# Kernel optimization log

Measured on AMD Instinct MI355X. Metric: run time of the kernel, lower is better.

## Reference

```python
import jax, jax.numpy as jnp
import numpy as np
import math

N_AGENTS = 16

def _mlp2(x, W1, b1, W2, b2):
    # tanh on first layer only, matching the torch module
    return jnp.tanh(x @ W1 + b1) @ W2 + b2

def setup_inputs() -> dict:
    key = jax.random.key(0)
    ks = jax.random.split(key, 24)
    B, N, A, IN, D = 2048, N_AGENTS, 32, 128, 128
    NODES = B * N
    s = 0.05
    inp = {
        "obs": jax.random.normal(ks[0], (NODES, IN), jnp.float32),
        "policies": jax.random.uniform(ks[1], (NODES, A), jnp.float32),
        "actions": jax.random.uniform(ks[2], (NODES, A), jnp.float32),
        "weights": jax.random.uniform(ks[3], (1,), jnp.float32),
        "noise": jax.random.normal(ks[4], (NODES, N, A), jnp.float32) * 0.1,
        "Wk1": jax.random.normal(ks[5], (IN, 32), jnp.float32) * s,
        "bk1": jnp.zeros((32,), jnp.float32),
        "Wk2": jax.random.normal(ks[6], (32, D), jnp.float32) * s,
        "bk2": jnp.zeros((D,), jnp.float32),
        "Wq1": jax.random.normal(ks[7], (IN, 32), jnp.float32) * s,
        "bq1": jnp.zeros((32,), jnp.float32),
        "Wq2": jax.random.normal(ks[8], (32, D), jnp.float32) * s,
        "bq2": jnp.zeros((D,), jnp.float32),
        "Wv1": jax.random.normal(ks[9], (IN, 32), jnp.float32) * s,
        "bv1": jnp.zeros((32,), jnp.float32),
        "Wv2": jax.random.normal(ks[10], (32, D), jnp.float32) * s,
        "bv2": jnp.zeros((D,), jnp.float32),
        "Wval": jax.random.normal(ks[11], (D + A, 1), jnp.float32) * s,
        "bval": jnp.zeros((1,), jnp.float32),
    }
    return inp

def reference(obs, policies, actions, weights, noise,
              Wk1, bk1, Wk2, bk2, Wq1, bq1, Wq2, bq2, Wv1, bv1, Wv2, bv2,
              Wval, bval):
    N = N_AGENTS
    NODES, _ = obs.shape
    B = NODES // N
    A = policies.shape[-1]
    D = Wk2.shape[1]

    # ---- SoftAttentionInput: graph soft attention over complete N-agent graphs
    k = _mlp2(obs, Wk1, bk1, Wk2, bk2).reshape(B, N, D)
    q = _mlp2(obs, Wq1, bq1, Wq2, bq2).reshape(B, N, D)
    v = _mlp2(obs, Wv1, bv1, Wv2, bv2).reshape(B, N, D)
    # score for receiver i from sender j: key[j] . query[i]
    scores = jnp.einsum('bjd,bid->bij', k, q) / math.sqrt(D)
    alpha = jax.nn.softmax(scores, axis=-1)               # softmax over senders j
    obs_proc = jnp.einsum('bij,bjd->bid', alpha, v)       # [B,N,D]

    # ---- SoftAttentionWeight: PRD mixing of policies and noisy actions
    pi = policies.reshape(B, N, A)
    act = actions.reshape(B, N, A)
    w = weights                                           # scalar mixing weight, shape (1,)
    # z[b,i,k] = w*act[b,k] + (1-w)*pi[b,k] + noise (mailbox of receiver i)
    z = w * act[:, None, :, :] + (1.0 - w) * pi[:, None, :, :] + noise.reshape(B, N, N, A)
    # place_policies construction: z_final[b,i,j,k] = pi[b,k] if k==j else z[b,i,k];
    # mean over k  =>  (pi[b,j] - z[b,i,j] + sum_k z[b,i,k]) / N
    z_sum = jnp.sum(z, axis=2)                            # [B,N,A]
    z_mix = (pi[:, None, :, :] - z + z_sum[:, :, None, :]) / N  # [B,i,j,A]

    obs_b = jnp.broadcast_to(obs_proc[:, None, :, :], (B, N, N, D))  # [b,i,j] = obs_proc[b,j]
    obs_final = jnp.concatenate([obs_b, z_mix], axis=-1).reshape(B * N, N, D + A)

    # ---- ValueNetwork
    x = obs_final @ Wval + bval                           # [B*N, N, 1]
    weights_preproc = alpha.reshape(B * N, N, 1)
    return x, weights_preproc
```

## Files before the change

### kernel.cpp

```cpp
#include <hip/hip_runtime.h>

typedef __attribute__((ext_vector_type(8))) short bf16x8;
typedef __attribute__((ext_vector_type(4))) float f32x4;

__device__ __forceinline__ unsigned short f2bf(float f){
  union { float f; unsigned int u; } v; v.f = f;
  unsigned int u = v.u;
  return (unsigned short)((u + 0x7FFFu + ((u >> 16) & 1u)) >> 16);
}

__device__ __forceinline__ float fast_tanh(float x){
  x = fminf(15.f, fmaxf(-15.f, x));
  float e = __expf(2.f * x);
  return (e - 1.f) / (e + 1.f);
}

__device__ __forceinline__ float dot128(const float* __restrict__ a,
                                        const float* __restrict__ b){
  float s = 0.f;
  for (int c = 0; c < 128; c += 4){
    float4 x = *(const float4*)(a + c);
    float4 y = *(const float4*)(b + c);
    s += x.x*y.x + x.y*y.y + x.z*y.z + x.w*y.w;
  }
  return s;
}

#define GRPSUM(x) { x += __shfl_xor(x, 1); x += __shfl_xor(x, 2); \
                    x += __shfl_xor(x, 4); x += __shfl_xor(x, 8); }

__global__ __launch_bounds__(64) void k0_kernel(
    const float* __restrict__ Wk1, const float* __restrict__ Wq1, const float* __restrict__ Wv1,
    const float* __restrict__ Wk2, const float* __restrict__ bk2,
    const float* __restrict__ Wq2, const float* __restrict__ bq2,
    const float* __restrict__ Wv2, const float* __restrict__ bv2,
    const float* __restrict__ Wval, float* __restrict__ ws)
{
  const int tid = blockIdx.x * 64 + threadIdx.x;
  const float rs = 0.08838834764831845f;
  unsigned short* bp = (unsigned short*)ws;
  unsigned short* b2 = (unsigned short*)(ws + 6144);

  if (tid < 1536){
    const int e = tid & 7, l = (tid >> 3) & 63, tt = tid >> 9;
    const int g = (l >> 4) * 8 + e;
    float val = 0.f;
    if (tt < 2){
      const int h = (l & 15) + tt * 16;
      val = rs * dot128(Wk2 + h * 128, Wq2 + g * 128);
    } else if ((l & 15) == 0){
      val = rs * dot128(Wq2 + g * 128, bk2);
    }
    b2[tid] = f2bf(val);
  } else if (tid < 1600){
    const int h = tid - 1536;
    if (h < 32) ws[6912 + h] = rs * dot128(Wk2 + h * 128, bq2);
    else        ws[6944 + (h - 32)] = dot128(Wv2 + (h - 32) * 128, Wval);
  } else if (tid == 1600){
    ws[6976] = rs * dot128(bk2, bq2);
  } else if (tid == 1601){
    ws[6977] = dot128(bv2, Wval);
  }

  for (int idx = tid; idx < 12288; idx += 4096){
    const int e  = idx & 7;
    const int l  = (idx >> 3) & 63;
    const int kc = (idx >> 9) & 3;
    const int nt = (idx >> 11) & 1;
    const int m  = idx >> 12;
    const float* W1 = (m == 0) ? Wk1 : ((m == 1) ? Wq1 : Wv1);
    const int krow = kc * 32 + (l >> 4) * 8 + e;
    const int col  = nt * 16 + (l & 15);
    bp[idx] = f2bf(W1[krow * 32 + col]);
  }
}

__global__ __launch_bounds__(256, 2) void fused_kernel(
    const float* __restrict__ obs,
    const float* __restrict__ policies, const float* __restrict__ actions,
    const float* __restrict__ noise, const float* __restrict__ weights,
    const float* __restrict__ bk1p, const float* __restrict__ bq1p, const float* __restrict__ bv1p,
    const float* __restrict__ Wval, const float* __restrict__ bval,
    const float* __restrict__ ws,
    float* __restrict__ out_x, float* __restrict__ out_alpha)
{
  __shared__ __align__(16) unsigned short hk_s[4][512];
  __shared__ __align__(16) unsigned short hq_s[4][512];
  __shared__ __align__(16) unsigned short tq_s[4][512];
  __shared__ __align__(16) float rql_s[4][16];
  __shared__ __align__(16) float vvl_s[4][16];
  __shared__ __align__(16) float nvw_s[4][256];
  __shared__ __align__(16) float pvl_s[4][16], avl_s[4][16], ovl_s[4][16];

  const int t = threadIdx.x;
  const int wid = t >> 6, l = t & 63;
  const int b = blockIdx.x * 4 + wid;
  const int li = l & 15, gp = l >> 4;

  const float* orow = obs + (size_t)(b * 16 + li) * 128 + gp * 8;
  float4 ob[8];
#pragma unroll
  for (int kc = 0; kc < 4; kc++){
    ob[kc * 2]     = *(const float4*)(orow + kc * 32);
    ob[kc * 2 + 1] = *(const float4*)(orow + kc * 32 + 4);
  }

  const int q8 = l & 7, r8 = l >> 3;
  const float* nb = noise + (size_t)b * 8192 + r8 * 32 + q8 * 4;
  float4 nzA[8], nzB[8];
#pragma unroll
  for (int p = 0; p < 8; p++) nzA[p] = *(const float4*)(nb + p * 256);

  const int jp = l >> 2, seg = l & 3;
  const float* pp = policies + (size_t)(b * 16 + jp) * 32 + seg * 8;
  const float* ap = actions  + (size_t)(b * 16 + jp) * 32 + seg * 8;
  float4 pA0 = *(const float4*)(pp);
  float4 pA1 = *(const float4*)(pp + 4);
  float4 aA0 = *(const float4*)(ap);
  float4 aA1 = *(const float4*)(ap + 4);
  const float4 wpa = *(const float4*)(Wval + 128 + seg * 8);
  const float4 wpb = *(const float4*)(Wval + 132 + seg * 8);
  const float4 wv4 = *(const float4*)(Wval + 128 + q8 * 4);

  const bf16x8* bp  = (const bf16x8*)ws;
  const bf16x8* b2p = (const bf16x8*)(ws + 6144);
  const bf16x8 b20 = b2p[l], b21 = b2p[64 + l], b22 = b2p[128 + l];
  const float u0 = ws[6912 + li], u1 = ws[6928 + li];
  const float wv0 = ws[6944 + li], wv1 = ws[6960 + li];
  const float ccv = ws[6976], cvv = ws[6977];
  const float bk0 = bk1p[li], bk1v = bk1p[16 + li];
  const float bq0 = bq1p[li], bq1v = bq1p[16 + li];
  const float bv0 = bv1p[li], bv1v = bv1p[16 + li];
  const float wscal = weights[0];
  const float bvs = bval[0];

  bf16x8 afr[4];
#pragma unroll
  for (int kc = 0; kc < 4; kc++){
    bf16x8 a;
    a[0]=(short)f2bf(ob[kc*2].x); a[1]=(short)f2bf(ob[kc*2].y);
    a[2]=(short)f2bf(ob[kc*2].z); a[3]=(short)f2bf(ob[kc*2].w);
    a[4]=(short)f2bf(ob[kc*2+1].x); a[5]=(short)f2bf(ob[kc*2+1].y);
    a[6]=(short)f2bf(ob[kc*2+1].z); a[7]=(short)f2bf(ob[kc*2+1].w);
    afr[kc] = a;
  }
  f32x4 acc[6];
#pragma unroll
  for (int mt = 0; mt < 6; mt++){ f32x4 z = {0.f,0.f,0.f,0.f}; acc[mt] = z; }
#pragma unroll
  for (int mt = 0; mt < 6; mt++){
#pragma unroll
    for (int kc = 0; kc < 4; kc++)
      acc[mt] = __builtin_amdgcn_mfma_f32_16x16x32_bf16(afr[kc], bp[(mt*4+kc)*64 + l], acc[mt], 0, 0, 0);
  }

  unsigned short* hkb = hk_s[wid];
  unsigned short* hqb = hq_s[wid];
#pragma unroll
  for (int tile = 0; tile < 2; tile++){
    const float bk_ = tile ? bk1v : bk0;
    const float bq_ = tile ? bq1v : bq0;
    f32x4 ck = acc[tile], cq = acc[2 + tile];
#pragma unroll
    for (int r = 0; r < 4; r++){
      hkb[(gp*4+r)*32 + tile*16 + li] = f2bf(fast_tanh(ck[r] + bk_));
      hqb[(gp*4+r)*32 + tile*16 + li] = f2bf(fast_tanh(cq[r] + bq_));
    }
  }

  {
    f32x4 c0 = acc[4], c1 = acc[5];
    float vp0 = wv0*fast_tanh(c0[0]+bv0) + wv1*fast_tanh(c1[0]+bv1v);
    float vp1 = wv0*fast_tanh(c0[1]+bv0) + wv1*fast_tanh(c1[1]+bv1v);
    float vp2 = wv0*fast_tanh(c0[2]+bv0) + wv1*fast_tanh(c1[2]+bv1v);
    float vp3 = wv0*fast_tanh(c0[3]+bv0) + wv1*fast_tanh(c1[3]+bv1v);
    GRPSUM(vp0); GRPSUM(vp1); GRPSUM(vp2); GRPSUM(vp3);
    if (li == 0){
      float4 vq; vq.x = vp0+cvv; vq.y = vp1+cvv; vq.z = vp2+cvv; vq.w = vp3+cvv;
      *(float4*)&vvl_s[wid][gp*4] = vq;
    }
  }

#pragma unroll
  for (int p = 0; p < 8; p++) nzB[p] = *(const float4*)(nb + 2048 + p * 256);
  float* nvw = nvw_s[wid];
#pragma unroll
  for (int p = 0; p < 8; p++){
    float s = nzA[p].x*wv4.x + nzA[p].y*wv4.y + nzA[p].z*wv4.z + nzA[p].w*wv4.w;
    s += __shfl_xor(s, 1); s += __shfl_xor(s, 2); s += __shfl_xor(s, 4);
    if (q8 == 0) nvw[p * 8 + r8] = s;
  }
#pragma unroll
  for (int p = 0; p < 8; p++) nzA[p] = *(const float4*)(nb + 4096 + p * 256);

  const bf16x8 aq = *(const bf16x8*)(hqb + li*32 + gp*8);
  f32x4 cu0 = {u0,u0,u0,u0}, cu1 = {u1,u1,u1,u1}, cu2 = {ccv,ccv,ccv,ccv};
  f32x4 tq0 = __builtin_amdgcn_mfma_f32_16x16x32_bf16(aq, b20, cu0, 0, 0, 0);
  f32x4 tq1 = __builtin_amdgcn_mfma_f32_16x16x32_bf16(aq, b21, cu1, 0, 0, 0);
  f32x4 rqt = __builtin_amdgcn_mfma_f32_16x16x32_bf16(aq, b22, cu2, 0, 0, 0);
  if (li == 0){
    float4 rv; rv.x = rqt[0]; rv.y = rqt[1]; rv.z = rqt[2]; rv.w = rqt[3];
    *(float4*)&rql_s[wid][gp*4] = rv;
  }
  unsigned short* tqb = tq_s[wid];
#pragma unroll
  for (int r = 0; r < 4; r++){
    tqb[(gp*4+r)*32 + li]      = f2bf(tq0[r]);
    tqb[(gp*4+r)*32 + 16 + li] = f2bf(tq1[r]);
  }

  const bf16x8 ak = *(const bf16x8*)(hkb + li*32 + gp*8);
  const bf16x8 bt = *(const bf16x8*)(tqb + li*32 + gp*8);
  f32x4 zz = {0.f,0.f,0.f,0.f};
  f32x4 S = __builtin_amdgcn_mfma_f32_16x16x32_bf16(ak, bt, zz, 0, 0, 0);
  const float rc = rql_s[wid][li];
  float s0 = S[0]+rc, s1 = S[1]+rc, s2 = S[2]+rc, s3 = S[3]+rc;

  float mx = fmaxf(fmaxf(s0, s1), fmaxf(s2, s3));
  mx = fmaxf(mx, __shfl_xor(mx, 16)); mx = fmaxf(mx, __shfl_xor(mx, 32));
  float e0 = __expf(s0-mx), e1 = __expf(s1-mx), e2 = __expf(s2-mx), e3 = __expf(s3-mx);
  float sm = e0+e1+e2+e3;
  sm += __shfl_xor(sm, 16); sm += __shfl_xor(sm, 32);
  const float inv = 1.f / sm;
  const float a0 = e0*inv, a1 = e1*inv, a2 = e2*inv, a3 = e3*inv;

  float* aT = (float*)tqb;
  { float4 av4; av4.x = a0; av4.y = a1; av4.z = a2; av4.w = a3;
    *(float4*)&aT[li*16 + gp*4] = av4; }
  { float4 o4 = *(const float4*)&aT[l*4];
    *(float4*)(out_alpha + (size_t)b*256 + l*4) = o4; }

  float4 vq4 = *(const float4*)&vvl_s[wid][gp*4];
  float ovp = a0*vq4.x + a1*vq4.y + a2*vq4.z + a3*vq4.w;
  ovp += __shfl_xor(ovp, 16); ovp += __shfl_xor(ovp, 32);
  if (l < 16) ovl_s[wid][li] = ovp;

#pragma unroll
  for (int p = 0; p < 8; p++){
    float s = nzB[p].x*wv4.x + nzB[p].y*wv4.y + nzB[p].z*wv4.z + nzB[p].w*wv4.w;
    s += __shfl_xor(s, 1); s += __shfl_xor(s, 2); s += __shfl_xor(s, 4);
    if (q8 == 0) nvw[64 + p * 8 + r8] = s;
  }
#pragma unroll
  for (int p = 0; p < 8; p++) nzB[p] = *(const float4*)(nb + 6144 + p * 256);

  {
    float pvv = pA0.x*wpa.x + pA0.y*wpa.y + pA0.z*wpa.z + pA0.w*wpa.w
              + pA1.x*wpb.x + pA1.y*wpb.y + pA1.z*wpb.z + pA1.w*wpb.w;
    float avv = aA0.x*wpa.x + aA0.y*wpa.y + aA0.z*wpa.z + aA0.w*wpa.w
              + aA1.x*wpb.x + aA1.y*wpb.y + aA1.z*wpb.z + aA1.w*wpb.w;
    pvv += __shfl_xor(pvv, 1); pvv += __shfl_xor(pvv, 2);
    avv += __shfl_xor(avv, 1); avv += __shfl_xor(avv, 2);
    if (seg == 0){ pvl_s[wid][jp] = pvv; avl_s[wid][jp] = avv; }
  }

#pragma unroll
  for (int p = 0; p < 8; p++){
    float s = nzA[p].x*wv4.x + nzA[p].y*wv4.y + nzA[p].z*wv4.z + nzA[p].w*wv4.w;
    s += __shfl_xor(s, 1); s += __shfl_xor(s, 2); s += __shfl_xor(s, 4);
    if (q8 == 0) nvw[128 + p * 8 + r8] = s;
  }
#pragma unroll
  for (int p = 0; p < 8; p++){
    float s = nzB[p].x*wv4.x + nzB[p].y*wv4.y + nzB[p].z*wv4.z + nzB[p].w*wv4.w;
    s += __shfl_xor(s, 1); s += __shfl_xor(s, 2); s += __shfl_xor(s, 4);
    if (q8 == 0) nvw[192 + p * 8 + r8] = s;
  }

  {
    const int j0 = (l & 3) * 4;
    const int ii = l >> 2;
    float4 pv4 = *(const float4*)&pvl_s[wid][j0];
    float4 av4 = *(const float4*)&avl_s[wid][j0];
    float4 ov4 = *(const float4*)&ovl_s[wid][j0];
    float4 nv4 = *(const float4*)&nvw[ii * 16 + j0];
    const float om = 1.f - wscal;
    float z0 = wscal * av4.x + om * pv4.x + nv4.x;
    float z1 = wscal * av4.y + om * pv4.y + nv4.y;
    float z2 = wscal * av4.z + om * pv4.z + nv4.z;
    float z3 = wscal * av4.w + om * pv4.w + nv4.w;
    float zs = z0 + z1 + z2 + z3;
    zs += __shfl_xor(zs, 1); zs += __shfl_xor(zs, 2);
    float4 o;
    o.x = ov4.x + (pv4.x - z0 + zs) * 0.0625f + bvs;
    o.y = ov4.y + (pv4.y - z1 + zs) * 0.0625f + bvs;
    o.z = ov4.z + (pv4.z - z2 + zs) * 0.0625f + bvs;
    o.w = ov4.w + (pv4.w - z3 + zs) * 0.0625f + bvs;
    *(float4*)(out_x + (size_t)b * 256 + l * 4) = o;
  }
}

extern "C" void kernel_launch(void* const* d_in, const int* in_sizes, int n_in,
                              void* d_out, int out_size, void* d_ws, size_t ws_size,
                              hipStream_t stream)
{
  const float* obs      = (const float*)d_in[0];
  const float* policies = (const float*)d_in[1];
  const float* actions  = (const float*)d_in[2];
  const float* weights  = (const float*)d_in[3];
  const float* noise    = (const float*)d_in[4];
  const float* Wk1  = (const float*)d_in[5];
  const float* bk1  = (const float*)d_in[6];
  const float* Wk2  = (const float*)d_in[7];
  const float* bk2  = (const float*)d_in[8];
  const float* Wq1  = (const float*)d_in[9];
  const float* bq1  = (const float*)d_in[10];
  const float* Wq2  = (const float*)d_in[11];
  const float* bq2  = (const float*)d_in[12];
  const float* Wv1  = (const float*)d_in[13];
  const float* bv1  = (const float*)d_in[14];
  const float* Wv2  = (const float*)d_in[15];
  const float* bv2  = (const float*)d_in[16];
  const float* Wval = (const float*)d_in[17];
  const float* bval = (const float*)d_in[18];

  float* out = (float*)d_out;
  float* ws  = (float*)d_ws;

  const int NODES = in_sizes[0] / 128;
  const int B = NODES / 16;

  float* out_x     = out;
  float* out_alpha = out + (size_t)NODES * 16;

  hipLaunchKernelGGL(k0_kernel, dim3(64), dim3(64), 0, stream,
                     Wk1, Wq1, Wv1, Wk2, bk2, Wq2, bq2, Wv2, bv2, Wval, ws);
  hipLaunchKernelGGL(fused_kernel, dim3(B / 4), dim3(256), 0, stream,
                     obs, policies, actions, noise, weights,
                     bk1, bq1, bv1, Wval, bval, ws,
                     out_x, out_alpha);
}
```

Measured before the change: 30.80 us.

## Split per-graph work across warps: one warp attention, three warps noise reduction

Rather than each warp handling a whole graph, one block now processes one graph. Warp 0 runs the MLP and attention MFMAs, while warps 1-3 share the noise-row dot products with Wval and the policy/action projections. A block barrier joins them before a 256-thread final combine. This raises the block count and spreads the noise-load latency, which dominates memory traffic, across more warps. The cost is an added __syncthreads and warp 0 now serialising its attention work against the others.

```diff
diff --git a/kernel.cpp b/kernel.cpp
--- a/kernel.cpp
+++ b/kernel.cpp
@@ -75,7 +75,7 @@
   }
 }
 
-__global__ __launch_bounds__(256, 2) void fused_kernel(
+__global__ __launch_bounds__(256, 2) void fused2_kernel(
     const float* __restrict__ obs,
     const float* __restrict__ policies, const float* __restrict__ actions,
     const float* __restrict__ noise, const float* __restrict__ weights,
@@ -84,209 +84,182 @@
     const float* __restrict__ ws,
     float* __restrict__ out_x, float* __restrict__ out_alpha)
 {
-  __shared__ __align__(16) unsigned short hk_s[4][512];
-  __shared__ __align__(16) unsigned short hq_s[4][512];
-  __shared__ __align__(16) unsigned short tq_s[4][512];
-  __shared__ __align__(16) float rql_s[4][16];
-  __shared__ __align__(16) float vvl_s[4][16];
-  __shared__ __align__(16) float nvw_s[4][256];
-  __shared__ __align__(16) float pvl_s[4][16], avl_s[4][16], ovl_s[4][16];
+  __shared__ __align__(16) unsigned short hk_s[512];
+  __shared__ __align__(16) unsigned short hq_s[512];
+  __shared__ __align__(16) unsigned short tq_s[512];
+  __shared__ __align__(16) float rql_s[16];
+  __shared__ __align__(16) float vvl_s[16];
+  __shared__ __align__(16) float nvw[256];
+  __shared__ __align__(16) float pvl_s[16], avl_s[16], ovl_s[16];
 
   const int t = threadIdx.x;
   const int wid = t >> 6, l = t & 63;
-  const int b = blockIdx.x * 4 + wid;
-  const int li = l & 15, gp = l >> 4;
-
-  const float* orow = obs + (size_t)(b * 16 + li) * 128 + gp * 8;
-  float4 ob[8];
-#pragma unroll
-  for (int kc = 0; kc < 4; kc++){
-    ob[kc * 2]     = *(const float4*)(orow + kc * 32);
-    ob[kc * 2 + 1] = *(const float4*)(orow + kc * 32 + 4);
-  }
-
-  const int q8 = l & 7, r8 = l >> 3;
-  const float* nb = noise + (size_t)b * 8192 + r8 * 32 + q8 * 4;
-  float4 nzA[8], nzB[8];
-#pragma unroll
-  for (int p = 0; p < 8; p++) nzA[p] = *(const float4*)(nb + p * 256);
-
-  const int jp = l >> 2, seg = l & 3;
-  const float* pp = policies + (size_t)(b * 16 + jp) * 32 + seg * 8;
-  const float* ap = actions  + (size_t)(b * 16 + jp) * 32 + seg * 8;
-  float4 pA0 = *(const float4*)(pp);
-  float4 pA1 = *(const float4*)(pp + 4);
-  float4 aA0 = *(const float4*)(ap);
-  float4 aA1 = *(const float4*)(ap + 4);
-  const float4 wpa = *(const float4*)(Wval + 128 + seg * 8);
-  const float4 wpb = *(const float4*)(Wval + 132 + seg * 8);
-  const float4 wv4 = *(const float4*)(Wval + 128 + q8 * 4);
-
-  const bf16x8* bp  = (const bf16x8*)ws;
-  const bf16x8* b2p = (const bf16x8*)(ws + 6144);
-  const bf16x8 b20 = b2p[l], b21 = b2p[64 + l], b22 = b2p[128 + l];
-  const float u0 = ws[6912 + li], u1 = ws[6928 + li];
-  const float wv0 = ws[6944 + li], wv1 = ws[6960 + li];
-  const float ccv = ws[6976], cvv = ws[6977];
-  const float bk0 = bk1p[li], bk1v = bk1p[16 + li];
-  const float bq0 = bq1p[li], bq1v = bq1p[16 + li];
-  const float bv0 = bv1p[li], bv1v = bv1p[16 + li];
+  const int b = blockIdx.x;
   const float wscal = weights[0];
   const float bvs = bval[0];
 
-  bf16x8 afr[4];
-#pragma unroll
-  for (int kc = 0; kc < 4; kc++){
-    bf16x8 a;
-    a[0]=(short)f2bf(ob[kc*2].x); a[1]=(short)f2bf(ob[kc*2].y);
-    a[2]=(short)f2bf(ob[kc*2].z); a[3]=(short)f2bf(ob[kc*2].w);
-    a[4]=(short)f2bf(ob[kc*2+1].x); a[5]=(short)f2bf(ob[kc*2+1].y);
-    a[6]=(short)f2bf(ob[kc*2+1].z); a[7]=(short)f2bf(ob[kc*2+1].w);
-    afr[kc] = a;
-  }
-  f32x4 acc[6];
-#pragma unroll
-  for (int mt = 0; mt < 6; mt++){ f32x4 z = {0.f,0.f,0.f,0.f}; acc[mt] = z; }
-#pragma unroll
-  for (int mt = 0; mt < 6; mt++){
-#pragma unroll
-    for (int kc = 0; kc < 4; kc++)
-      acc[mt] = __builtin_amdgcn_mfma_f32_16x16x32_bf16(afr[kc], bp[(mt*4+kc)*64 + l], acc[mt], 0, 0, 0);
-  }
-
-  unsigned short* hkb = hk_s[wid];
-  unsigned short* hqb = hq_s[wid];
-#pragma unroll
-  for (int tile = 0; tile < 2; tile++){
-    const float bk_ = tile ? bk1v : bk0;
-    const float bq_ = tile ? bq1v : bq0;
-    f32x4 ck = acc[tile], cq = acc[2 + tile];
+  if (wid == 0){
+    const int li = l & 15, gp = l >> 4;
+
+    const float* orow = obs + (size_t)(b * 16 + li) * 128 + gp * 8;
+    float4 ob[8];
+#pragma unroll
+    for (int kc = 0; kc < 4; kc++){
+      ob[kc * 2]     = *(const float4*)(orow + kc * 32);
+      ob[kc * 2 + 1] = *(const float4*)(orow + kc * 32 + 4);
+    }
+
+    const bf16x8* bp  = (const bf16x8*)ws;
+    const bf16x8* b2p = (const bf16x8*)(ws + 6144);
+    const bf16x8 b20 = b2p[l], b21 = b2p[64 + l], b22 = b2p[128 + l];
+    const float u0 = ws[6912 + li], u1 = ws[6928 + li];
+    const float wv0 = ws[6944 + li], wv1 = ws[6960 + li];
+    const float ccv = ws[6976], cvv = ws[6977];
+    const float bk0 = bk1p[li], bk1v = bk1p[16 + li];
+    const float bq0 = bq1p[li], bq1v = bq1p[16 + li];
+    const float bv0 = bv1p[li], bv1v = bv1p[16 + li];
+
+    bf16x8 afr[4];
+#pragma unroll
+    for (int kc = 0; kc < 4; kc++){
+      bf16x8 a;
+      a[0]=(short)f2bf(ob[kc*2].x); a[1]=(short)f2bf(ob[kc*2].y);
+      a[2]=(short)f2bf(ob[kc*2].z); a[3]=(short)f2bf(ob[kc*2].w);
+      a[4]=(short)f2bf(ob[kc*2+1].x); a[5]=(short)f2bf(ob[kc*2+1].y);
+      a[6]=(short)f2bf(ob[kc*2+1].z); a[7]=(short)f2bf(ob[kc*2+1].w);
+      afr[kc] = a;
+    }
+    f32x4 acc[6];
+#pragma unroll
+    for (int mt = 0; mt < 6; mt++){ f32x4 z = {0.f,0.f,0.f,0.f}; acc[mt] = z; }
+#pragma unroll
+    for (int mt = 0; mt < 6; mt++){
+#pragma unroll
+      for (int kc = 0; kc < 4; kc++)
+        acc[mt] = __builtin_amdgcn_mfma_f32_16x16x32_bf16(afr[kc], bp[(mt*4+kc)*64 + l], acc[mt], 0, 0, 0);
+    }
+
+#pragma unroll
+    for (int tile = 0; tile < 2; tile++){
+      const float bk_ = tile ? bk1v : bk0;
+      const float bq_ = tile ? bq1v : bq0;
+      f32x4 ck = acc[tile], cq = acc[2 + tile];
+#pragma unroll
+      for (int r = 0; r < 4; r++){
+        hk_s[(gp*4+r)*32 + tile*16 + li] = f2bf(fast_tanh(ck[r] + bk_));
+        hq_s[(gp*4+r)*32 + tile*16 + li] = f2bf(fast_tanh(cq[r] + bq_));
+      }
+    }
+
+    {
+      f32x4 c0 = acc[4], c1 = acc[5];
+      float vp0 = wv0*fast_tanh(c0[0]+bv0) + wv1*fast_tanh(c1[0]+bv1v);
+      float vp1 = wv0*fast_tanh(c0[1]+bv0) + wv1*fast_tanh(c1[1]+bv1v);
+      float vp2 = wv0*fast_tanh(c0[2]+bv0) + wv1*fast_tanh(c1[2]+bv1v);
+      float vp3 = wv0*fast_tanh(c0[3]+bv0) + wv1*fast_tanh(c1[3]+bv1v);
+      GRPSUM(vp0); GRPSUM(vp1); GRPSUM(vp2); GRPSUM(vp3);
+      if (li == 0){
+        float4 vq; vq.x = vp0+cvv; vq.y = vp1+cvv; vq.z = vp2+cvv; vq.w = vp3+cvv;
+        *(float4*)&vvl_s[gp*4] = vq;
+      }
+    }
+
+    const bf16x8 aq = *(const bf16x8*)(hq_s + li*32 + gp*8);
+    f32x4 cu0 = {u0,u0,u0,u0}, cu1 = {u1,u1,u1,u1}, cu2 = {ccv,ccv,ccv,ccv};
+    f32x4 tq0 = __builtin_amdgcn_mfma_f32_16x16x32_bf16(aq, b20, cu0, 0, 0, 0);
+    f32x4 tq1 = __builtin_amdgcn_mfma_f32_16x16x32_bf16(aq, b21, cu1, 0, 0, 0);
+    f32x4 rqt = __builtin_amdgcn_mfma_f32_16x16x32_bf16(aq, b22, cu2, 0, 0, 0);
+    if (li == 0){
+      float4 rv; rv.x = rqt[0]; rv.y = rqt[1]; rv.z = rqt[2]; rv.w = rqt[3];
+      *(float4*)&rql_s[gp*4] = rv;
+    }
 #pragma unroll
     for (int r = 0; r < 4; r++){
-      hkb[(gp*4+r)*32 + tile*16 + li] = f2bf(fast_tanh(ck[r] + bk_));
-      hqb[(gp*4+r)*32 + tile*16 + li] = f2bf(fast_tanh(cq[r] + bq_));
-    }
-  }
+      tq_s[(gp*4+r)*32 + li]      = f2bf(tq0[r]);
+      tq_s[(gp*4+r)*32 + 16 + li] = f2bf(tq1[r]);
+    }
+
+    const bf16x8 ak = *(const bf16x8*)(hk_s + li*32 + gp*8);
+    const bf16x8 bt = *(const bf16x8*)(tq_s + li*32 + gp*8);
+    f32x4 zz = {0.f,0.f,0.f,0.f};
+    f32x4 S = __builtin_amdgcn_mfma_f32_16x16x32_bf16(ak, bt, zz, 0, 0, 0);
+    const float rc = rql_s[li];
+    float s0 = S[0]+rc, s1 = S[1]+rc, s2 = S[2]+rc, s3 = S[3]+rc;
+
+    float mx = fmaxf(fmaxf(s0, s1), fmaxf(s2, s3));
+    mx = fmaxf(mx, __shfl_xor(mx, 16)); mx = fmaxf(mx, __shfl_xor(mx, 32));
+    float e0 = __expf(s0-mx), e1 = __expf(s1-mx), e2 = __expf(s2-mx), e3 = __expf(s3-mx);
+    float sm = e0+e1+e2+e3;
+    sm += __shfl_xor(sm, 16); sm += __shfl_xor(sm, 32);
+    const float inv = 1.f / sm;
+    const float a0 = e0*inv, a1 = e1*inv, a2 = e2*inv, a3 = e3*inv;
+
+    float* aT = (float*)tq_s;
+    { float4 av4; av4.x = a0; av4.y = a1; av4.z = a2; av4.w = a3;
+      *(float4*)&aT[li*16 + gp*4] = av4; }
+    { float4 o4 = *(const float4*)&aT[l*4];
+      *(float4*)(out_alpha + (size_t)b*256 + l*4) = o4; }
+
+    float4 vq4 = *(const float4*)&vvl_s[gp*4];
+    float ovp = a0*vq4.x + a1*vq4.y + a2*vq4.z + a3*vq4.w;
+    ovp += __shfl_xor(ovp, 16); ovp += __shfl_xor(ovp, 32);
+    if (l < 16) ovl_s[l] = ovp;
+  } else {
+    const int wn = wid - 1;
+    const int q8 = l & 7, r8 = l >> 3;
+    const int rbase = wn * 88 + r8;
+    const float* nb = noise + (size_t)b * 8192;
+    const float4 wv4 = *(const float4*)(Wval + 128 + q8 * 4);
+
+    float4 pA0, pA1, aA0, aA1, wpa, wpb;
+    const int jp = l >> 2, seg = l & 3;
+    if (wid == 1){
+      const float* pp = policies + (size_t)(b * 16 + jp) * 32 + seg * 8;
+      const float* ap = actions  + (size_t)(b * 16 + jp) * 32 + seg * 8;
+      pA0 = *(const float4*)(pp);
+      pA1 = *(const float4*)(pp + 4);
+      aA0 = *(const float4*)(ap);
+      aA1 = *(const float4*)(ap + 4);
+      wpa = *(const float4*)(Wval + 128 + seg * 8);
+      wpb = *(const float4*)(Wval + 132 + seg * 8);
+    }
+
+    float4 nz[11];
+#pragma unroll
+    for (int p = 0; p < 11; p++){
+      const int row = rbase + p * 8;
+      if (row < 256) nz[p] = *(const float4*)(nb + row * 32 + q8 * 4);
+    }
+#pragma unroll
+    for (int p = 0; p < 11; p++){
+      const int row = rbase + p * 8;
+      if (row < 256){
+        float s = nz[p].x*wv4.x + nz[p].y*wv4.y + nz[p].z*wv4.z + nz[p].w*wv4.w;
+        s += __shfl_xor(s, 1); s += __shfl_xor(s, 2); s += __shfl_xor(s, 4);
+        if (q8 == 0) nvw[row] = s;
+      }
+    }
+
+    if (wid == 1){
+      float pvv = pA0.x*wpa.x + pA0.y*wpa.y + pA0.z*wpa.z + pA0.w*wpa.w
+                + pA1.x*wpb.x + pA1.y*wpb.y + pA1.z*wpb.z + pA1.w*wpb.w;
+      float avv = aA0.x*wpa.x + aA0.y*wpa.y + aA0.z*wpa.z + aA0.w*wpa.w
+                + aA1.x*wpb.x + aA1.y*wpb.y + aA1.z*wpb.z + aA1.w*wpb.w;
+      pvv += __shfl_xor(pvv, 1); pvv += __shfl_xor(pvv, 2);
+      avv += __shfl_xor(avv, 1); avv += __shfl_xor(avv, 2);
+      if (seg == 0){ pvl_s[jp] = pvv; avl_s[jp] = avv; }
+    }
+  }
+
+  __syncthreads();
 
   {
-    f32x4 c0 = acc[4], c1 = acc[5];
-    float vp0 = wv0*fast_tanh(c0[0]+bv0) + wv1*fast_tanh(c1[0]+bv1v);
-    float vp1 = wv0*fast_tanh(c0[1]+bv0) + wv1*fast_tanh(c1[1]+bv1v);
-    float vp2 = wv0*fast_tanh(c0[2]+bv0) + wv1*fast_tanh(c1[2]+bv1v);
-    float vp3 = wv0*fast_tanh(c0[3]+bv0) + wv1*fast_tanh(c1[3]+bv1v);
-    GRPSUM(vp0); GRPSUM(vp1); GRPSUM(vp2); GRPSUM(vp3);
-    if (li == 0){
-      float4 vq; vq.x = vp0+cvv; vq.y = vp1+cvv; vq.z = vp2+cvv; vq.w = vp3+cvv;
-      *(float4*)&vvl_s[wid][gp*4] = vq;
-    }
-  }
-
-#pragma unroll
-  for (int p = 0; p < 8; p++) nzB[p] = *(const float4*)(nb + 2048 + p * 256);
-  float* nvw = nvw_s[wid];
-#pragma unroll
-  for (int p = 0; p < 8; p++){
-    float s = nzA[p].x*wv4.x + nzA[p].y*wv4.y + nzA[p].z*wv4.z + nzA[p].w*wv4.w;
-    s += __shfl_xor(s, 1); s += __shfl_xor(s, 2); s += __shfl_xor(s, 4);
-    if (q8 == 0) nvw[p * 8 + r8] = s;
-  }
-#pragma unroll
-  for (int p = 0; p < 8; p++) nzA[p] = *(const float4*)(nb + 4096 + p * 256);
-
-  const bf16x8 aq = *(const bf16x8*)(hqb + li*32 + gp*8);
-  f32x4 cu0 = {u0,u0,u0,u0}, cu1 = {u1,u1,u1,u1}, cu2 = {ccv,ccv,ccv,ccv};
-  f32x4 tq0 = __builtin_amdgcn_mfma_f32_16x16x32_bf16(aq, b20, cu0, 0, 0, 0);
-  f32x4 tq1 = __builtin_amdgcn_mfma_f32_16x16x32_bf16(aq, b21, cu1, 0, 0, 0);
-  f32x4 rqt = __builtin_amdgcn_mfma_f32_16x16x32_bf16(aq, b22, cu2, 0, 0, 0);
-  if (li == 0){
-    float4 rv; rv.x = rqt[0]; rv.y = rqt[1]; rv.z = rqt[2]; rv.w = rqt[3];
-    *(float4*)&rql_s[wid][gp*4] = rv;
-  }
-  unsigned short* tqb = tq_s[wid];
-#pragma unroll
-  for (int r = 0; r < 4; r++){
-    tqb[(gp*4+r)*32 + li]      = f2bf(tq0[r]);
-    tqb[(gp*4+r)*32 + 16 + li] = f2bf(tq1[r]);
-  }
-
-  const bf16x8 ak = *(const bf16x8*)(hkb + li*32 + gp*8);
-  const bf16x8 bt = *(const bf16x8*)(tqb + li*32 + gp*8);
-  f32x4 zz = {0.f,0.f,0.f,0.f};
-  f32x4 S = __builtin_amdgcn_mfma_f32_16x16x32_bf16(ak, bt, zz, 0, 0, 0);
-  const float rc = rql_s[wid][li];
-  float s0 = S[0]+rc, s1 = S[1]+rc, s2 = S[2]+rc, s3 = S[3]+rc;
-
-  float mx = fmaxf(fmaxf(s0, s1), fmaxf(s2, s3));
-  mx = fmaxf(mx, __shfl_xor(mx, 16)); mx = fmaxf(mx, __shfl_xor(mx, 32));
-  float e0 = __expf(s0-mx), e1 = __expf(s1-mx), e2 = __expf(s2-mx), e3 = __expf(s3-mx);
-  float sm = e0+e1+e2+e3;
-  sm += __shfl_xor(sm, 16); sm += __shfl_xor(sm, 32);
-  const float inv = 1.f / sm;
-  const float a0 = e0*inv, a1 = e1*inv, a2 = e2*inv, a3 = e3*inv;
-
-  float* aT = (float*)tqb;
-  { float4 av4; av4.x = a0; av4.y = a1; av4.z = a2; av4.w = a3;
-    *(float4*)&aT[li*16 + gp*4] = av4; }
-  { float4 o4 = *(const float4*)&aT[l*4];
-    *(float4*)(out_alpha + (size_t)b*256 + l*4) = o4; }
-
-  float4 vq4 = *(const float4*)&vvl_s[wid][gp*4];
-  float ovp = a0*vq4.x + a1*vq4.y + a2*vq4.z + a3*vq4.w;
-  ovp += __shfl_xor(ovp, 16); ovp += __shfl_xor(ovp, 32);
-  if (l < 16) ovl_s[wid][li] = ovp;
-
-#pragma unroll
-  for (int p = 0; p < 8; p++){
-    float s = nzB[p].x*wv4.x + nzB[p].y*wv4.y + nzB[p].z*wv4.z + nzB[p].w*wv4.w;
-    s += __shfl_xor(s, 1); s += __shfl_xor(s, 2); s += __shfl_xor(s, 4);
-    if (q8 == 0) nvw[64 + p * 8 + r8] = s;
-  }
-#pragma unroll
-  for (int p = 0; p < 8; p++) nzB[p] = *(const float4*)(nb + 6144 + p * 256);
-
-  {
-    float pvv = pA0.x*wpa.x + pA0.y*wpa.y + pA0.z*wpa.z + pA0.w*wpa.w
-              + pA1.x*wpb.x + pA1.y*wpb.y + pA1.z*wpb.z + pA1.w*wpb.w;
-    float avv = aA0.x*wpa.x + aA0.y*wpa.y + aA0.z*wpa.z + aA0.w*wpa.w
-              + aA1.x*wpb.x + aA1.y*wpb.y + aA1.z*wpb.z + aA1.w*wpb.w;
-    pvv += __shfl_xor(pvv, 1); pvv += __shfl_xor(pvv, 2);
-    avv += __shfl_xor(avv, 1); avv += __shfl_xor(avv, 2);
-    if (seg == 0){ pvl_s[wid][jp] = pvv; avl_s[wid][jp] = avv; }
-  }
-
-#pragma unroll
-  for (int p = 0; p < 8; p++){
-    float s = nzA[p].x*wv4.x + nzA[p].y*wv4.y + nzA[p].z*wv4.z + nzA[p].w*wv4.w;
-    s += __shfl_xor(s, 1); s += __shfl_xor(s, 2); s += __shfl_xor(s, 4);
-    if (q8 == 0) nvw[128 + p * 8 + r8] = s;
-  }
-#pragma unroll
-  for (int p = 0; p < 8; p++){
-    float s = nzB[p].x*wv4.x + nzB[p].y*wv4.y + nzB[p].z*wv4.z + nzB[p].w*wv4.w;
-    s += __shfl_xor(s, 1); s += __shfl_xor(s, 2); s += __shfl_xor(s, 4);
-    if (q8 == 0) nvw[192 + p * 8 + r8] = s;
-  }
-
-  {
-    const int j0 = (l & 3) * 4;
-    const int ii = l >> 2;
-    float4 pv4 = *(const float4*)&pvl_s[wid][j0];
-    float4 av4 = *(const float4*)&avl_s[wid][j0];
-    float4 ov4 = *(const float4*)&ovl_s[wid][j0];
-    float4 nv4 = *(const float4*)&nvw[ii * 16 + j0];
-    const float om = 1.f - wscal;
-    float z0 = wscal * av4.x + om * pv4.x + nv4.x;
-    float z1 = wscal * av4.y + om * pv4.y + nv4.y;
-    float z2 = wscal * av4.z + om * pv4.z + nv4.z;
-    float z3 = wscal * av4.w + om * pv4.w + nv4.w;
-    float zs = z0 + z1 + z2 + z3;
-    zs += __shfl_xor(zs, 1); zs += __shfl_xor(zs, 2);
-    float4 o;
-    o.x = ov4.x + (pv4.x - z0 + zs) * 0.0625f + bvs;
-    o.y = ov4.y + (pv4.y - z1 + zs) * 0.0625f + bvs;
-    o.z = ov4.z + (pv4.z - z2 + zs) * 0.0625f + bvs;
-    o.w = ov4.w + (pv4.w - z3 + zs) * 0.0625f + bvs;
-    *(float4*)(out_x + (size_t)b * 256 + l * 4) = o;
+    const int j = t & 15;
+    const float pv = pvl_s[j], av = avl_s[j];
+    const float zval = wscal * av + (1.f - wscal) * pv + nvw[t];
+    float zs = zval;
+    GRPSUM(zs);
+    out_x[(size_t)b * 256 + t] = ovl_s[t >> 4] + (pv - zval + zs) * 0.0625f + bvs;
   }
 }
 
@@ -325,7 +298,7 @@
 
   hipLaunchKernelGGL(k0_kernel, dim3(64), dim3(64), 0, stream,
                      Wk1, Wq1, Wv1, Wk2, bk2, Wq2, bq2, Wv2, bv2, Wval, ws);
-  hipLaunchKernelGGL(fused_kernel, dim3(B / 4), dim3(256), 0, stream,
+  hipLaunchKernelGGL(fused2_kernel, dim3(B), dim3(256), 0, stream,
                      obs, policies, actions, noise, weights,
                      bk1, bq1, bv1, Wval, bval, ws,
                      out_x, out_alpha);
```

Measured after the change: 32.02 us. 4.0% more time.

## Split noise/policy mixing into separate wide kernel, attention kernel adds onto output

Applied to the files above, without the earlier changes.

Moves the noise reduction and policy/action mixing part of the value output out of the fused attention kernel into the prologue kernel. That kernel now launches one 256-thread block per batch (plus four weight-prep blocks). The attention kernel then reads the partial output and adds the attention-value term. This spreads the bandwidth-heavy noise streaming (the largest input) across many more blocks and cuts register pressure in the attention kernel. In exchange it adds an extra global write and read of out_x and makes the second kernel depend on the first one finishing.

```diff
diff --git a/kernel.cpp b/kernel.cpp
--- a/kernel.cpp
+++ b/kernel.cpp
@@ -29,58 +29,131 @@
 #define GRPSUM(x) { x += __shfl_xor(x, 1); x += __shfl_xor(x, 2); \
                     x += __shfl_xor(x, 4); x += __shfl_xor(x, 8); }
 
-__global__ __launch_bounds__(64) void k0_kernel(
+
+__global__ __launch_bounds__(256) void kn_kernel(
+    const float* __restrict__ policies, const float* __restrict__ actions,
+    const float* __restrict__ noise, const float* __restrict__ weights,
+    const float* __restrict__ Wval, const float* __restrict__ bval,
     const float* __restrict__ Wk1, const float* __restrict__ Wq1, const float* __restrict__ Wv1,
     const float* __restrict__ Wk2, const float* __restrict__ bk2,
     const float* __restrict__ Wq2, const float* __restrict__ bq2,
     const float* __restrict__ Wv2, const float* __restrict__ bv2,
-    const float* __restrict__ Wval, float* __restrict__ ws)
+    float* __restrict__ ws, float* __restrict__ out_x)
 {
-  const int tid = blockIdx.x * 64 + threadIdx.x;
-  const float rs = 0.08838834764831845f;
-  unsigned short* bp = (unsigned short*)ws;
-  unsigned short* b2 = (unsigned short*)(ws + 6144);
-
-  if (tid < 1536){
-    const int e = tid & 7, l = (tid >> 3) & 63, tt = tid >> 9;
-    const int g = (l >> 4) * 8 + e;
-    float val = 0.f;
-    if (tt < 2){
-      const int h = (l & 15) + tt * 16;
-      val = rs * dot128(Wk2 + h * 128, Wq2 + g * 128);
-    } else if ((l & 15) == 0){
-      val = rs * dot128(Wq2 + g * 128, bk2);
+  const int t = threadIdx.x;
+
+  if ((int)blockIdx.x < 4){
+    const int tid2 = blockIdx.x * 256 + t;
+    const float rs = 0.08838834764831845f;
+    unsigned short* bp = (unsigned short*)ws;
+    unsigned short* b2 = (unsigned short*)(ws + 6144);
+
+    for (int d = tid2; d < 1602; d += 1024){
+      if (d < 1536){
+        const int e = d & 7, l = (d >> 3) & 63, tt = d >> 9;
+        const int g = (l >> 4) * 8 + e;
+        float val = 0.f;
+        if (tt < 2){
+          const int h = (l & 15) + tt * 16;
+          val = rs * dot128(Wk2 + h * 128, Wq2 + g * 128);
+        } else if ((l & 15) == 0){
+          val = rs * dot128(Wq2 + g * 128, bk2);
+        }
+        b2[d] = f2bf(val);
+      } else if (d < 1600){
+        const int h = d - 1536;
+        if (h < 32) ws[6912 + h] = rs * dot128(Wk2 + h * 128, bq2);
+        else        ws[6944 + (h - 32)] = dot128(Wv2 + (h - 32) * 128, Wval);
+      } else if (d == 1600){
+        ws[6976] = rs * dot128(bk2, bq2);
+      } else {
+        ws[6977] = dot128(bv2, Wval);
+      }
     }
-    b2[tid] = f2bf(val);
-  } else if (tid < 1600){
-    const int h = tid - 1536;
-    if (h < 32) ws[6912 + h] = rs * dot128(Wk2 + h * 128, bq2);
-    else        ws[6944 + (h - 32)] = dot128(Wv2 + (h - 32) * 128, Wval);
-  } else if (tid == 1600){
-    ws[6976] = rs * dot128(bk2, bq2);
-  } else if (tid == 1601){
-    ws[6977] = dot128(bv2, Wval);
-  }
-
-  for (int idx = tid; idx < 12288; idx += 4096){
-    const int e  = idx & 7;
-    const int l  = (idx >> 3) & 63;
-    const int kc = (idx >> 9) & 3;
-    const int nt = (idx >> 11) & 1;
-    const int m  = idx >> 12;
-    const float* W1 = (m == 0) ? Wk1 : ((m == 1) ? Wq1 : Wv1);
-    const int krow = kc * 32 + (l >> 4) * 8 + e;
-    const int col  = nt * 16 + (l & 15);
-    bp[idx] = f2bf(W1[krow * 32 + col]);
-  }
-}
-
-__global__ __launch_bounds__(256, 2) void fused_kernel(
+    for (int idx = tid2; idx < 12288; idx += 1024){
+      const int e  = idx & 7;
+      const int l  = (idx >> 3) & 63;
+      const int kc = (idx >> 9) & 3;
+      const int nt = (idx >> 11) & 1;
+      const int m  = idx >> 12;
+      const float* W1 = (m == 0) ? Wk1 : ((m == 1) ? Wq1 : Wv1);
+      const int krow = kc * 32 + (l >> 4) * 8 + e;
+      const int col  = nt * 16 + (l & 15);
+      bp[idx] = f2bf(W1[krow * 32 + col]);
+    }
+    return;
+  }
+
+  __shared__ __align__(16) float nvw[256];
+  __shared__ __align__(16) float pvl[16], avl[16];
+
+  const int b = blockIdx.x - 4;
+  const int w = t >> 6, l = t & 63;
+  const int q8 = l & 7, r8 = l >> 3;
+  const float4 wv4 = *(const float4*)(Wval + 128 + q8 * 4);
+
+  float4 pA0, pA1, aA0, aA1, wpa, wpb;
+  const int jp = l >> 2, seg = l & 3;
+  if (w == 0){
+    const float* pp = policies + (size_t)(b * 16 + jp) * 32 + seg * 8;
+    const float* ap = actions  + (size_t)(b * 16 + jp) * 32 + seg * 8;
+    pA0 = *(const float4*)(pp);
+    pA1 = *(const float4*)(pp + 4);
+    aA0 = *(const float4*)(ap);
+    aA1 = *(const float4*)(ap + 4);
+    wpa = *(const float4*)(Wval + 128 + seg * 8);
+    wpb = *(const float4*)(Wval + 132 + seg * 8);
+  }
+
+  const float* nbl = noise + (size_t)b * 8192 + (w * 64 + r8) * 32 + q8 * 4;
+  float4 nz[8];
+#pragma unroll
+  for (int p = 0; p < 8; p++) nz[p] = *(const float4*)(nbl + p * 256);
+#pragma unroll
+  for (int p = 0; p < 8; p++){
+    float s = nz[p].x*wv4.x + nz[p].y*wv4.y + nz[p].z*wv4.z + nz[p].w*wv4.w;
+    s += __shfl_xor(s, 1); s += __shfl_xor(s, 2); s += __shfl_xor(s, 4);
+    if (q8 == 0) nvw[w * 64 + p * 8 + r8] = s;
+  }
+
+  if (w == 0){
+    float pvv = pA0.x*wpa.x + pA0.y*wpa.y + pA0.z*wpa.z + pA0.w*wpa.w
+              + pA1.x*wpb.x + pA1.y*wpb.y + pA1.z*wpb.z + pA1.w*wpb.w;
+    float avv = aA0.x*wpa.x + aA0.y*wpa.y + aA0.z*wpa.z + aA0.w*wpa.w
+              + aA1.x*wpb.x + aA1.y*wpb.y + aA1.z*wpb.z + aA1.w*wpb.w;
+    pvv += __shfl_xor(pvv, 1); pvv += __shfl_xor(pvv, 2);
+    avv += __shfl_xor(avv, 1); avv += __shfl_xor(avv, 2);
+    if (seg == 0){ pvl[jp] = pvv; avl[jp] = avv; }
+  }
+
+  __syncthreads();
+
+  if (w == 0){
+    const float wscal = weights[0];
+    const float bvs = bval[0];
+    const int i = l >> 2, j0 = (l & 3) * 4;
+    float4 pv4 = *(const float4*)&pvl[j0];
+    float4 av4 = *(const float4*)&avl[j0];
+    float4 nv4 = *(const float4*)&nvw[i * 16 + j0];
+    const float om = 1.f - wscal;
+    float z0 = wscal * av4.x + om * pv4.x + nv4.x;
+    float z1 = wscal * av4.y + om * pv4.y + nv4.y;
+    float z2 = wscal * av4.z + om * pv4.z + nv4.z;
+    float z3 = wscal * av4.w + om * pv4.w + nv4.w;
+    float zs = z0 + z1 + z2 + z3;
+    zs += __shfl_xor(zs, 1); zs += __shfl_xor(zs, 2);
+    float4 o;
+    o.x = (pv4.x - z0 + zs) * 0.0625f + bvs;
+    o.y = (pv4.y - z1 + zs) * 0.0625f + bvs;
+    o.z = (pv4.z - z2 + zs) * 0.0625f + bvs;
+    o.w = (pv4.w - z3 + zs) * 0.0625f + bvs;
+    *(float4*)(out_x + (size_t)b * 256 + l * 4) = o;
+  }
+}
+
+__global__ __launch_bounds__(256) void ka_kernel(
     const float* __restrict__ obs,
-    const float* __restrict__ policies, const float* __restrict__ actions,
-    const float* __restrict__ noise, const float* __restrict__ weights,
     const float* __restrict__ bk1p, const float* __restrict__ bq1p, const float* __restrict__ bv1p,
-    const float* __restrict__ Wval, const float* __restrict__ bval,
     const float* __restrict__ ws,
     float* __restrict__ out_x, float* __restrict__ out_alpha)
 {
@@ -89,8 +162,7 @@
   __shared__ __align__(16) unsigned short tq_s[4][512];
   __shared__ __align__(16) float rql_s[4][16];
   __shared__ __align__(16) float vvl_s[4][16];
-  __shared__ __align__(16) float nvw_s[4][256];
-  __shared__ __align__(16) float pvl_s[4][16], avl_s[4][16], ovl_s[4][16];
+  __shared__ __align__(16) float ovl_s[4][16];
 
   const int t = threadIdx.x;
   const int wid = t >> 6, l = t & 63;
@@ -104,23 +176,7 @@
     ob[kc * 2]     = *(const float4*)(orow + kc * 32);
     ob[kc * 2 + 1] = *(const float4*)(orow + kc * 32 + 4);
   }
-
-  const int q8 = l & 7, r8 = l >> 3;
-  const float* nb = noise + (size_t)b * 8192 + r8 * 32 + q8 * 4;
-  float4 nzA[8], nzB[8];
-#pragma unroll
-  for (int p = 0; p < 8; p++) nzA[p] = *(const float4*)(nb + p * 256);
-
-  const int jp = l >> 2, seg = l & 3;
-  const float* pp = policies + (size_t)(b * 16 + jp) * 32 + seg * 8;
-  const float* ap = actions  + (size_t)(b * 16 + jp) * 32 + seg * 8;
-  float4 pA0 = *(const float4*)(pp);
-  float4 pA1 = *(const float4*)(pp + 4);
-  float4 aA0 = *(const float4*)(ap);
-  float4 aA1 = *(const float4*)(ap + 4);
-  const float4 wpa = *(const float4*)(Wval + 128 + seg * 8);
-  const float4 wpb = *(const float4*)(Wval + 132 + seg * 8);
-  const float4 wv4 = *(const float4*)(Wval + 128 + q8 * 4);
+  float4 x4 = *(const float4*)(out_x + (size_t)b * 256 + l * 4);
 
   const bf16x8* bp  = (const bf16x8*)ws;
   const bf16x8* b2p = (const bf16x8*)(ws + 6144);
@@ -131,8 +187,6 @@
   const float bk0 = bk1p[li], bk1v = bk1p[16 + li];
   const float bq0 = bq1p[li], bq1v = bq1p[16 + li];
   const float bv0 = bv1p[li], bv1v = bv1p[16 + li];
-  const float wscal = weights[0];
-  const float bvs = bval[0];
 
   bf16x8 afr[4];
 #pragma unroll
@@ -181,18 +235,6 @@
     }
   }
 
-#pragma unroll
-  for (int p = 0; p < 8; p++) nzB[p] = *(const float4*)(nb + 2048 + p * 256);
-  float* nvw = nvw_s[wid];
-#pragma unroll
-  for (int p = 0; p < 8; p++){
-    float s = nzA[p].x*wv4.x + nzA[p].y*wv4.y + nzA[p].z*wv4.z + nzA[p].w*wv4.w;
-    s += __shfl_xor(s, 1); s += __shfl_xor(s, 2); s += __shfl_xor(s, 4);
-    if (q8 == 0) nvw[p * 8 + r8] = s;
-  }
-#pragma unroll
-  for (int p = 0; p < 8; p++) nzA[p] = *(const float4*)(nb + 4096 + p * 256);
-
   const bf16x8 aq = *(const bf16x8*)(hqb + li*32 + gp*8);
   f32x4 cu0 = {u0,u0,u0,u0}, cu1 = {u1,u1,u1,u1}, cu2 = {ccv,ccv,ccv,ccv};
   f32x4 tq0 = __builtin_amdgcn_mfma_f32_16x16x32_bf16(aq, b20, cu0, 0, 0, 0);
@@ -233,60 +275,12 @@
   float4 vq4 = *(const float4*)&vvl_s[wid][gp*4];
   float ovp = a0*vq4.x + a1*vq4.y + a2*vq4.z + a3*vq4.w;
   ovp += __shfl_xor(ovp, 16); ovp += __shfl_xor(ovp, 32);
-  if (l < 16) ovl_s[wid][li] = ovp;
-
-#pragma unroll
-  for (int p = 0; p < 8; p++){
-    float s = nzB[p].x*wv4.x + nzB[p].y*wv4.y + nzB[p].z*wv4.z + nzB[p].w*wv4.w;
-    s += __shfl_xor(s, 1); s += __shfl_xor(s, 2); s += __shfl_xor(s, 4);
-    if (q8 == 0) nvw[64 + p * 8 + r8] = s;
-  }
-#pragma unroll
-  for (int p = 0; p < 8; p++) nzB[p] = *(const float4*)(nb + 6144 + p * 256);
+  if (l < 16) ovl_s[wid][l] = ovp;
 
   {
-    float pvv = pA0.x*wpa.x + pA0.y*wpa.y + pA0.z*wpa.z + pA0.w*wpa.w
-              + pA1.x*wpb.x + pA1.y*wpb.y + pA1.z*wpb.z + pA1.w*wpb.w;
-    float avv = aA0.x*wpa.x + aA0.y*wpa.y + aA0.z*wpa.z + aA0.w*wpa.w
-              + aA1.x*wpb.x + aA1.y*wpb.y + aA1.z*wpb.z + aA1.w*wpb.w;
-    pvv += __shfl_xor(pvv, 1); pvv += __shfl_xor(pvv, 2);
-    avv += __shfl_xor(avv, 1); avv += __shfl_xor(avv, 2);
-    if (seg == 0){ pvl_s[wid][jp] = pvv; avl_s[wid][jp] = avv; }
-  }
-
-#pragma unroll
-  for (int p = 0; p < 8; p++){
-    float s = nzA[p].x*wv4.x + nzA[p].y*wv4.y + nzA[p].z*wv4.z + nzA[p].w*wv4.w;
-    s += __shfl_xor(s, 1); s += __shfl_xor(s, 2); s += __shfl_xor(s, 4);
-    if (q8 == 0) nvw[128 + p * 8 + r8] = s;
-  }
-#pragma unroll
-  for (int p = 0; p < 8; p++){
-    float s = nzB[p].x*wv4.x + nzB[p].y*wv4.y + nzB[p].z*wv4.z + nzB[p].w*wv4.w;
-    s += __shfl_xor(s, 1); s += __shfl_xor(s, 2); s += __shfl_xor(s, 4);
-    if (q8 == 0) nvw[192 + p * 8 + r8] = s;
-  }
-
-  {
-    const int j0 = (l & 3) * 4;
-    const int ii = l >> 2;
-    float4 pv4 = *(const float4*)&pvl_s[wid][j0];
-    float4 av4 = *(const float4*)&avl_s[wid][j0];
-    float4 ov4 = *(const float4*)&ovl_s[wid][j0];
-    float4 nv4 = *(const float4*)&nvw[ii * 16 + j0];
-    const float om = 1.f - wscal;
-    float z0 = wscal * av4.x + om * pv4.x + nv4.x;
-    float z1 = wscal * av4.y + om * pv4.y + nv4.y;
-    float z2 = wscal * av4.z + om * pv4.z + nv4.z;
-    float z3 = wscal * av4.w + om * pv4.w + nv4.w;
-    float zs = z0 + z1 + z2 + z3;
-    zs += __shfl_xor(zs, 1); zs += __shfl_xor(zs, 2);
-    float4 o;
-    o.x = ov4.x + (pv4.x - z0 + zs) * 0.0625f + bvs;
-    o.y = ov4.y + (pv4.y - z1 + zs) * 0.0625f + bvs;
-    o.z = ov4.z + (pv4.z - z2 + zs) * 0.0625f + bvs;
-    o.w = ov4.w + (pv4.w - z3 + zs) * 0.0625f + bvs;
-    *(float4*)(out_x + (size_t)b * 256 + l * 4) = o;
+    float4 ov4 = *(const float4*)&ovl_s[wid][(l & 3) * 4];
+    x4.x += ov4.x; x4.y += ov4.y; x4.z += ov4.z; x4.w += ov4.w;
+    *(float4*)(out_x + (size_t)b * 256 + l * 4) = x4;
   }
 }
 
@@ -323,10 +317,10 @@
   float* out_x     = out;
   float* out_alpha = out + (size_t)NODES * 16;
 
-  hipLaunchKernelGGL(k0_kernel, dim3(64), dim3(64), 0, stream,
-                     Wk1, Wq1, Wv1, Wk2, bk2, Wq2, bq2, Wv2, bv2, Wval, ws);
-  hipLaunchKernelGGL(fused_kernel, dim3(B / 4), dim3(256), 0, stream,
-                     obs, policies, actions, noise, weights,
-                     bk1, bq1, bv1, Wval, bval, ws,
-                     out_x, out_alpha);
-}
+  hipLaunchKernelGGL(kn_kernel, dim3(B + 4), dim3(256), 0, stream,
+                     policies, actions, noise, weights, Wval, bval,
+                     Wk1, Wq1, Wv1, Wk2, bk2, Wq2, bq2, Wv2, bv2,
+                     ws, out_x);
+  hipLaunchKernelGGL(ka_kernel, dim3(B / 4), dim3(256), 0, stream,
+                     obs, bk1, bq1, bv1, ws, out_x, out_alpha);
+}
```

Result: faster. 29.22 us (-5.1%).
